# Kernel optimization log

Hardware: AMD Instinct MI355X
Metric: run time of the kernel (lower is better)

Reference implementation:

```python
import jax, jax.numpy as jnp
import numpy as np

VOCAB = 67
EMB = 32
BRANCH = 32
OUT = 96
L = 16
B = 131072


def setup_inputs() -> dict:
    key = jax.random.key(0)
    ks = jax.random.split(key, 10)
    x = jax.random.randint(ks[0], (B, L), 0, VOCAB, dtype=jnp.int64)
    embed = jax.random.normal(ks[1], (VOCAB, EMB), dtype=jnp.float32) * 0.1
    w2 = jax.random.normal(ks[2], (BRANCH, EMB, 2), dtype=jnp.float32) * 0.1
    b2 = jnp.zeros((BRANCH,), jnp.float32)
    w3 = jax.random.normal(ks[3], (BRANCH, EMB, 3), dtype=jnp.float32) * 0.1
    b3 = jnp.zeros((BRANCH,), jnp.float32)
    w4 = jax.random.normal(ks[4], (BRANCH, EMB, 4), dtype=jnp.float32) * 0.1
    b4 = jnp.zeros((BRANCH,), jnp.float32)
    pw = jax.random.normal(ks[5], (OUT, 3 * BRANCH), dtype=jnp.float32) * 0.02
    pb = jnp.zeros((OUT,), jnp.float32)
    return {"x": x, "embed": embed, "w2": w2, "b2": b2, "w3": w3,
            "b3": b3, "w4": w4, "b4": b4, "pw": pw, "pb": pb}


def _branch(emb_ncl, w, b):
    # emb_ncl: [B, EMB, L]; w: [BRANCH, EMB, k] -> conv valid, ReLU, max over time
    y = jax.lax.conv_general_dilated(
        emb_ncl, w, window_strides=(1,), padding='VALID',
        dimension_numbers=('NCH', 'OIH', 'NCH'))
    y = jax.nn.relu(y + b[None, :, None])
    return jnp.max(y, axis=2)  # [B, BRANCH]


def reference(x, embed, w2, b2, w3, b3, w4, b4, pw, pb):
    # padding_idx=0: row 0 of the table is zeros
    table = embed.at[0].set(0.0)
    emb = table[x]                      # [B, L, EMB]
    emb = jnp.transpose(emb, (0, 2, 1))  # [B, EMB, L]
    g2 = _branch(emb, w2, b2)
    g3 = _branch(emb, w3, b3)
    g4 = _branch(emb, w4, b4)
    feat = jnp.concatenate([g2, g3, g4], axis=1)  # [B, 96]
    # Linear + ReLU (dropout is identity at eval)
    return jax.nn.relu(feat @ pw.T + pb)
```

## Files before the change

kernel.cpp:

```cpp
#include <hip/hip_runtime.h>
#include <hip/hip_fp16.h>


#define VOCABSZ 67
#define EMBSZ   32
#define NCH     32
#define NFEAT   96
#define SEQL    16
#define BATCH   131072
#define NFP     (NFEAT / 2)
#define EMBW    1072
#define PWOFF_W EMBW
#define NPW     (NFEAT * NFP)
#define BFOFF_W (PWOFF_W + NPW)
#define NBF     18
#define WSW     (BFOFF_W + NBF * 256)
#define EMBLDS  (VOCABSZ * 128)
#define BFLDS   (NBF * 1024)
#define FBOFF   (EMBLDS + BFLDS)
#define FSTR    208
#define FBUF    (16 * FSTR)
#define LDSB    (FBOFF + 8 * FBUF)

typedef _Float16 v2h __attribute__((ext_vector_type(2)));
typedef _Float16 v8h __attribute__((ext_vector_type(8)));
typedef float    v4f __attribute__((ext_vector_type(4)));

__device__ __forceinline__ unsigned packh2(float a, float b) {
    v2h p; p[0] = (_Float16)a; p[1] = (_Float16)b;
    return __builtin_bit_cast(unsigned, p);
}

__global__ __launch_bounds__(256) void build_ws(
    const float* __restrict__ embed,
    const float* __restrict__ w2, const float* __restrict__ w3,
    const float* __restrict__ w4, const float* __restrict__ pw,
    unsigned* __restrict__ ws)
{
    int idx = blockIdx.x * 256 + threadIdx.x;
    if (idx < EMBW) {
        int v = idx >> 4, wd = idx & 15;
        int e0 = 2 * wd;
        ws[idx] = (v == 0) ? 0u
                : packh2(embed[v * EMBSZ + e0], embed[v * EMBSZ + e0 + 1]);
    } else if (idx < BFOFF_W) {
        int i  = idx - PWOFF_W;
        int o  = i / NFP;
        int fp = i - o * NFP;
        ws[idx] = packh2(pw[o * NFEAT + 2 * fp], pw[o * NFEAT + 2 * fp + 1]);
    } else if (idx < WSW) {
        int i    = idx - BFOFF_W;
        int fi   = i >> 8;
        int l    = (i >> 2) & 63;
        int wd   = i & 3;
        const float* w; int k, t, nt;
        if (fi < 4)       { w = w2; k = 2; t = fi >> 1;        nt = fi & 1; }
        else if (fi < 10) { w = w3; k = 3; t = (fi - 4) >> 1;  nt = (fi - 4) & 1; }
        else              { w = w4; k = 4; t = (fi - 10) >> 1; nt = (fi - 10) & 1; }
        int ch = 16 * nt + (l & 15);
        int e0 = 8 * (l >> 4) + 2 * wd;
        ws[idx] = packh2(w[(ch * EMBSZ + e0    ) * k + t],
                         w[(ch * EMBSZ + e0 + 1) * k + t]);
    }
}

template<int KT, int NP, int FI0, int CJ>
__device__ __forceinline__ void convmm(const v8h (&frag)[16],
                                       const char* __restrict__ lds,
                                       const float* __restrict__ bj,
                                       char* fb, int lane)
{
    const int nl = lane & 15, g = lane >> 4;
    #pragma unroll
    for (int nt = 0; nt < 2; ++nt) {
        float bv = bj[16 * nt + nl];
        v8h B[KT];
        #pragma unroll
        for (int t = 0; t < KT; ++t)
            B[t] = *reinterpret_cast<const v8h*>(
                lds + EMBLDS + (FI0 + 2 * t + nt) * 1024 + lane * 16);
        v4f mx = {0.f, 0.f, 0.f, 0.f};
        #pragma unroll
        for (int p = 0; p < NP; ++p) {
            v4f acc = {bv, bv, bv, bv};
            #pragma unroll
            for (int t = 0; t < KT; ++t)
                acc = __builtin_amdgcn_mfma_f32_16x16x32_f16(
                    frag[p + t], B[t], acc, 0, 0, 0);
            mx = __builtin_elementwise_max(mx, acc);
        }
        #pragma unroll
        for (int r = 0; r < 4; ++r)
            *reinterpret_cast<_Float16*>(
                fb + (4 * g + r) * FSTR + (CJ * 32 + 16 * nt + nl) * 2) =
                (_Float16)mx[r];
    }
}

__global__ __launch_bounds__(512, 2) void fused_cnn(
    const int*      __restrict__ x,
    const unsigned* __restrict__ ws,
    const float*    __restrict__ b2,
    const float*    __restrict__ b3,
    const float*    __restrict__ b4,
    const float*    __restrict__ pb,
    float*          __restrict__ out)
{
    extern __shared__ __align__(16) char lds[];
    const int tid  = threadIdx.x;
    const int lane = tid & 63;
    const int wv   = tid >> 6;
    const int ml   = lane & 15;
    const int c    = lane >> 4;
    const int parc = (((lane >> 3) & 1) << 6) + (c << 4);
    const int rowb = blockIdx.x * 128 + wv * 16;
    const int row  = rowb + ml;

    const int4* xp = reinterpret_cast<const int4*>(x + row * SEQL);
    int4 q0 = xp[0], q1 = xp[1], q2 = xp[2], q3 = xp[3];

    {
        const float4* s4 = reinterpret_cast<const float4*>(ws);
        float4* d4 = reinterpret_cast<float4*>(lds);
        if (tid < 268) {
            int v = tid >> 2, cw = tid & 3;
            float4 e = s4[tid];
            d4[v * 8 + cw]     = e;
            d4[v * 8 + 4 + cw] = e;
        }
        const float4* sb = reinterpret_cast<const float4*>(ws + BFOFF_W);
        float4* db = reinterpret_cast<float4*>(lds + EMBLDS);
        db[tid]       = sb[tid];
        db[tid + 512] = sb[tid + 512];
        if (tid < 128) db[tid + 1024] = sb[tid + 1024];
    }
    __syncthreads();

    char* fb = lds + FBOFF + wv * FBUF;

    int tq[16];
    tq[ 0] = q0.x; tq[ 1] = q0.y; tq[ 2] = q0.z; tq[ 3] = q0.w;
    tq[ 4] = q1.x; tq[ 5] = q1.y; tq[ 6] = q1.z; tq[ 7] = q1.w;
    tq[ 8] = q2.x; tq[ 9] = q2.y; tq[10] = q2.z; tq[11] = q2.w;
    tq[12] = q3.x; tq[13] = q3.y; tq[14] = q3.z; tq[15] = q3.w;

    v8h frag[16];
    #pragma unroll
    for (int q = 0; q < 16; ++q)
        frag[q] = *reinterpret_cast<const v8h*>(lds + (tq[q] << 7) + parc);

    convmm<2, 15,  0, 0>(frag, lds, b2, fb, lane);
    convmm<3, 14,  4, 1>(frag, lds, b3, fb, lane);
    convmm<4, 13, 10, 2>(frag, lds, b4, fb, lane);

    v8h m2 = *reinterpret_cast<const v8h*>(fb + ml * FSTR +       (c << 4));
    v8h m3 = *reinterpret_cast<const v8h*>(fb + ml * FSTR +  64 + (c << 4));
    v8h m4 = *reinterpret_cast<const v8h*>(fb + ml * FSTR + 128 + (c << 4));

    const unsigned* __restrict__ pwp = ws + PWOFF_W + ml * NFP + c * 4;
    #pragma unroll
    for (int u = 0; u < 6; ++u) {
        v4f acc = {0.f, 0.f, 0.f, 0.f};
        v8h w0 = *reinterpret_cast<const v8h*>(pwp + 768 * u);
        v8h w1 = *reinterpret_cast<const v8h*>(pwp + 768 * u + 16);
        v8h w2 = *reinterpret_cast<const v8h*>(pwp + 768 * u + 32);
        acc = __builtin_amdgcn_mfma_f32_16x16x32_f16(m2, w0, acc, 0, 0, 0);
        acc = __builtin_amdgcn_mfma_f32_16x16x32_f16(m3, w1, acc, 0, 0, 0);
        acc = __builtin_amdgcn_mfma_f32_16x16x32_f16(m4, w2, acc, 0, 0, 0);
        float pbl = pb[16 * u + ml];
        #pragma unroll
        for (int r = 0; r < 4; ++r)
            out[(size_t)(rowb + c * 4 + r) * NFEAT + 16 * u + ml] =
                fmaxf(acc[r] + pbl, 0.f);
    }
}

extern "C" void kernel_launch(void* const* d_in, const int* in_sizes, int n_in,
                              void* d_out, int out_size, void* d_ws, size_t ws_size,
                              hipStream_t stream)
{
    const int*   x     = (const int*)  d_in[0];
    const float* embed = (const float*)d_in[1];
    const float* w2    = (const float*)d_in[2];
    const float* b2    = (const float*)d_in[3];
    const float* w3    = (const float*)d_in[4];
    const float* b3    = (const float*)d_in[5];
    const float* w4    = (const float*)d_in[6];
    const float* b4    = (const float*)d_in[7];
    const float* pw    = (const float*)d_in[8];
    const float* pb    = (const float*)d_in[9];
    float* out = (float*)d_out;
    unsigned* ws = (unsigned*)d_ws;

    build_ws<<<(WSW + 255) / 256, 256, 0, stream>>>(embed, w2, w3, w4, pw, ws);

    fused_cnn<<<BATCH / 128, 512, LDSB, stream>>>(x, ws, b2, b3, b4, pb, out);
}
```

Baseline: 42.20 us.

## Add lookup-table conv path via precomputed vocab×weight products on alternate blocks

```diff
diff --git a/kernel.cpp b/kernel.cpp
--- a/kernel.cpp
+++ b/kernel.cpp
@@ -8,19 +8,23 @@
 #define NFEAT   96
 #define SEQL    16
 #define BATCH   131072
+#define NTAB    9
 #define NFP     (NFEAT / 2)
-#define EMBW    1072
-#define PWOFF_W EMBW
-#define NPW     (NFEAT * NFP)
-#define BFOFF_W (PWOFF_W + NPW)
+#define TABU    9648
+#define PWOFF   9648
+#define NPW     4608
+#define EMB_W   14256
+#define BFR_W   15328
 #define NBF     18
-#define WSW     (BFOFF_W + NBF * 256)
+#define WSW     19936
+#define ESTR    80
+#define LTS     (VOCABSZ * ESTR)
 #define EMBLDS  (VOCABSZ * 128)
 #define BFLDS   (NBF * 1024)
 #define FBOFF   (EMBLDS + BFLDS)
 #define FSTR    208
 #define FBUF    (16 * FSTR)
-#define LDSB    (FBOFF + 8 * FBUF)
+#define LDSB    53632
 
 typedef _Float16 v2h __attribute__((ext_vector_type(2)));
 typedef _Float16 v8h __attribute__((ext_vector_type(8)));
@@ -33,23 +37,47 @@
 
 __global__ __launch_bounds__(256) void build_ws(
     const float* __restrict__ embed,
-    const float* __restrict__ w2, const float* __restrict__ w3,
-    const float* __restrict__ w4, const float* __restrict__ pw,
+    const float* __restrict__ w2, const float* __restrict__ b2,
+    const float* __restrict__ w3, const float* __restrict__ b3,
+    const float* __restrict__ w4, const float* __restrict__ b4,
+    const float* __restrict__ pw,
     unsigned* __restrict__ ws)
 {
     int idx = blockIdx.x * 256 + threadIdx.x;
-    if (idx < EMBW) {
-        int v = idx >> 4, wd = idx & 15;
+    if (idx < TABU) {
+        int cp = idx & 15;
+        int t  = idx >> 4;
+        int j  = t / VOCABSZ;
+        int v  = t - j * VOCABSZ;
+        const float* w; const float* bias; int k, h;
+        if (j < 2)      { w = w2; k = 2; h = j;     bias = (h == 0) ? b2 : nullptr; }
+        else if (j < 5) { w = w3; k = 3; h = j - 2; bias = (h == 0) ? b3 : nullptr; }
+        else            { w = w4; k = 4; h = j - 5; bias = (h == 0) ? b4 : nullptr; }
+        int c0 = 2 * cp;
+        float a0 = bias ? bias[c0]     : 0.0f;
+        float a1 = bias ? bias[c0 + 1] : 0.0f;
+        if (v != 0) {
+            #pragma unroll
+            for (int e = 0; e < EMBSZ; ++e) {
+                float ev = embed[v * EMBSZ + e];
+                a0 += ev * w[((c0    ) * EMBSZ + e) * k + h];
+                a1 += ev * w[((c0 + 1) * EMBSZ + e) * k + h];
+            }
+        }
+        ws[t * 16 + cp] = packh2(a0, a1);
+    } else if (idx < EMB_W) {
+        int i  = idx - PWOFF;
+        int o  = i / NFP;
+        int fp = i - o * NFP;
+        ws[idx] = packh2(pw[o * NFEAT + 2 * fp], pw[o * NFEAT + 2 * fp + 1]);
+    } else if (idx < BFR_W) {
+        int i = idx - EMB_W;
+        int v = i >> 4, wd = i & 15;
         int e0 = 2 * wd;
         ws[idx] = (v == 0) ? 0u
                 : packh2(embed[v * EMBSZ + e0], embed[v * EMBSZ + e0 + 1]);
-    } else if (idx < BFOFF_W) {
-        int i  = idx - PWOFF_W;
-        int o  = i / NFP;
-        int fp = i - o * NFP;
-        ws[idx] = packh2(pw[o * NFEAT + 2 * fp], pw[o * NFEAT + 2 * fp + 1]);
     } else if (idx < WSW) {
-        int i    = idx - BFOFF_W;
+        int i    = idx - BFR_W;
         int fi   = i >> 8;
         int l    = (i >> 2) & 63;
         int wd   = i & 3;
@@ -97,7 +125,28 @@
     }
 }
 
-__global__ __launch_bounds__(512, 2) void fused_cnn(
+template<int K, int N, int P0, int TB>
+__device__ __forceinline__ void lconv(const char* __restrict__ base,
+                                      const int (&ap)[16], v8h& m)
+{
+    v8h s[N];
+    #pragma unroll
+    for (int u = 0; u < N; ++u)
+        s[u] = *reinterpret_cast<const v8h*>(base + TB + ap[P0 + u]);
+    #pragma unroll
+    for (int h = 1; h < K; ++h) {
+        v8h t[N];
+        #pragma unroll
+        for (int u = 0; u < N; ++u)
+            t[u] = *reinterpret_cast<const v8h*>(base + TB + h * LTS + ap[P0 + u + h]);
+        #pragma unroll
+        for (int u = 0; u < N; ++u) s[u] = s[u] + t[u];
+    }
+    #pragma unroll
+    for (int u = 0; u < N; ++u) m = __builtin_elementwise_max(m, s[u]);
+}
+
+__global__ __launch_bounds__(512, 4) void fused_cnn(
     const int*      __restrict__ x,
     const unsigned* __restrict__ ws,
     const float*    __restrict__ b2,
@@ -112,15 +161,15 @@
     const int wv   = tid >> 6;
     const int ml   = lane & 15;
     const int c    = lane >> 4;
-    const int parc = (((lane >> 3) & 1) << 6) + (c << 4);
     const int rowb = blockIdx.x * 128 + wv * 16;
     const int row  = rowb + ml;
+    const bool pathA = (blockIdx.x & 1) == 0;
 
     const int4* xp = reinterpret_cast<const int4*>(x + row * SEQL);
     int4 q0 = xp[0], q1 = xp[1], q2 = xp[2], q3 = xp[3];
 
-    {
-        const float4* s4 = reinterpret_cast<const float4*>(ws);
+    if (pathA) {
+        const float4* s4 = reinterpret_cast<const float4*>(ws + EMB_W);
         float4* d4 = reinterpret_cast<float4*>(lds);
         if (tid < 268) {
             int v = tid >> 2, cw = tid & 3;
@@ -128,36 +177,69 @@
             d4[v * 8 + cw]     = e;
             d4[v * 8 + 4 + cw] = e;
         }
-        const float4* sb = reinterpret_cast<const float4*>(ws + BFOFF_W);
+        const float4* sb = reinterpret_cast<const float4*>(ws + BFR_W);
         float4* db = reinterpret_cast<float4*>(lds + EMBLDS);
         db[tid]       = sb[tid];
         db[tid + 512] = sb[tid + 512];
         if (tid < 128) db[tid + 1024] = sb[tid + 1024];
+    } else {
+        const float4* s4 = reinterpret_cast<const float4*>(ws);
+        float4* d4 = reinterpret_cast<float4*>(lds);
+        #pragma unroll
+        for (int i0 = 0; i0 < 2560; i0 += 512) {
+            int i = i0 + tid;
+            if (i < 2412) {
+                int t = i >> 2, cc = i & 3;
+                d4[5 * t + cc] = s4[i];
+            }
+        }
     }
     __syncthreads();
 
-    char* fb = lds + FBOFF + wv * FBUF;
-
-    int tq[16];
-    tq[ 0] = q0.x; tq[ 1] = q0.y; tq[ 2] = q0.z; tq[ 3] = q0.w;
-    tq[ 4] = q1.x; tq[ 5] = q1.y; tq[ 6] = q1.z; tq[ 7] = q1.w;
-    tq[ 8] = q2.x; tq[ 9] = q2.y; tq[10] = q2.z; tq[11] = q2.w;
-    tq[12] = q3.x; tq[13] = q3.y; tq[14] = q3.z; tq[15] = q3.w;
-
-    v8h frag[16];
-    #pragma unroll
-    for (int q = 0; q < 16; ++q)
-        frag[q] = *reinterpret_cast<const v8h*>(lds + (tq[q] << 7) + parc);
-
-    convmm<2, 15,  0, 0>(frag, lds, b2, fb, lane);
-    convmm<3, 14,  4, 1>(frag, lds, b3, fb, lane);
-    convmm<4, 13, 10, 2>(frag, lds, b4, fb, lane);
-
-    v8h m2 = *reinterpret_cast<const v8h*>(fb + ml * FSTR +       (c << 4));
-    v8h m3 = *reinterpret_cast<const v8h*>(fb + ml * FSTR +  64 + (c << 4));
-    v8h m4 = *reinterpret_cast<const v8h*>(fb + ml * FSTR + 128 + (c << 4));
-
-    const unsigned* __restrict__ pwp = ws + PWOFF_W + ml * NFP + c * 4;
+    v8h m2, m3, m4;
+    if (pathA) {
+        const int parc = (((lane >> 3) & 1) << 6) + (c << 4);
+        char* fb = lds + FBOFF + wv * FBUF;
+        int tq[16];
+        tq[ 0] = q0.x; tq[ 1] = q0.y; tq[ 2] = q0.z; tq[ 3] = q0.w;
+        tq[ 4] = q1.x; tq[ 5] = q1.y; tq[ 6] = q1.z; tq[ 7] = q1.w;
+        tq[ 8] = q2.x; tq[ 9] = q2.y; tq[10] = q2.z; tq[11] = q2.w;
+        tq[12] = q3.x; tq[13] = q3.y; tq[14] = q3.z; tq[15] = q3.w;
+        v8h frag[16];
+        #pragma unroll
+        for (int q = 0; q < 16; ++q)
+            frag[q] = *reinterpret_cast<const v8h*>(lds + (tq[q] << 7) + parc);
+        convmm<2, 15,  0, 0>(frag, lds, b2, fb, lane);
+        convmm<3, 14,  4, 1>(frag, lds, b3, fb, lane);
+        convmm<4, 13, 10, 2>(frag, lds, b4, fb, lane);
+        m2 = *reinterpret_cast<const v8h*>(fb + ml * FSTR +       (c << 4));
+        m3 = *reinterpret_cast<const v8h*>(fb + ml * FSTR +  64 + (c << 4));
+        m4 = *reinterpret_cast<const v8h*>(fb + ml * FSTR + 128 + (c << 4));
+    } else {
+        const int co = c << 4;
+        int ap[16];
+        ap[ 0] = q0.x * ESTR + co; ap[ 1] = q0.y * ESTR + co;
+        ap[ 2] = q0.z * ESTR + co; ap[ 3] = q0.w * ESTR + co;
+        ap[ 4] = q1.x * ESTR + co; ap[ 5] = q1.y * ESTR + co;
+        ap[ 6] = q1.z * ESTR + co; ap[ 7] = q1.w * ESTR + co;
+        ap[ 8] = q2.x * ESTR + co; ap[ 9] = q2.y * ESTR + co;
+        ap[10] = q2.z * ESTR + co; ap[11] = q2.w * ESTR + co;
+        ap[12] = q3.x * ESTR + co; ap[13] = q3.y * ESTR + co;
+        ap[14] = q3.z * ESTR + co; ap[15] = q3.w * ESTR + co;
+        v8h a2 = {}, a3 = {}, a4 = {};
+        lconv<2, 5,  0, 0 * LTS>(lds, ap, a2);
+        lconv<2, 5,  5, 0 * LTS>(lds, ap, a2);
+        lconv<2, 5, 10, 0 * LTS>(lds, ap, a2);
+        lconv<3, 5,  0, 2 * LTS>(lds, ap, a3);
+        lconv<3, 5,  5, 2 * LTS>(lds, ap, a3);
+        lconv<3, 4, 10, 2 * LTS>(lds, ap, a3);
+        lconv<4, 5,  0, 5 * LTS>(lds, ap, a4);
+        lconv<4, 4,  5, 5 * LTS>(lds, ap, a4);
+        lconv<4, 4,  9, 5 * LTS>(lds, ap, a4);
+        m2 = a2; m3 = a3; m4 = a4;
+    }
+
+    const unsigned* __restrict__ pwp = ws + PWOFF + ml * NFP + c * 4;
     #pragma unroll
     for (int u = 0; u < 6; ++u) {
         v4f acc = {0.f, 0.f, 0.f, 0.f};
@@ -192,7 +274,11 @@
     float* out = (float*)d_out;
     unsigned* ws = (unsigned*)d_ws;
 
-    build_ws<<<(WSW + 255) / 256, 256, 0, stream>>>(embed, w2, w3, w4, pw, ws);
-
+    build_ws<<<(WSW + 255) / 256, 256, 0, stream>>>(
+        embed, w2, b2, w3, b3, w4, b4, pw, ws);
+
+    (void)hipFuncSetAttribute((const void*)fused_cnn,
+                              hipFuncAttributeMaxDynamicSharedMemorySize,
+                              LDSB);
     fused_cnn<<<BATCH / 128, 512, LDSB, stream>>>(x, ws, b2, b3, b4, pb, out);
 }
```

Result: slower. 43.08 us (+2.1%).
